# Kernel tuning notes

Hardware: AMD Instinct MI355X
Metric: run time of the kernel (lower is better)

## Reference

```python
import jax, jax.numpy as jnp
import numpy as np

N_NODES = 200_000
BRANCH = 8      # n: one-hot width / max children encoded
K_DEPTH = 16    # k: number of stacked levels, h_emb = n*k


def setup_inputs() -> dict:
    b, N = BRANCH, N_NODES
    idx = np.arange(N, dtype=np.int64)
    # complete b-ary forest (single tree): parent of node i is (i-1)//b
    parent = np.maximum((idx - 1) // b, 0)
    child_idx = np.where(idx > 0, (idx - 1) % b, 0)
    # depth via level start offsets of a complete b-ary tree
    starts = np.array([(b ** d - 1) // (b - 1) for d in range(K_DEPTH + 1)], dtype=np.int64)
    depth = (np.searchsorted(starts, idx, side='right') - 1).astype(np.int32)
    # p_emb buffer: p**i with p = 1.0 (unused by the original forward)
    p_emb = jnp.ones((BRANCH * K_DEPTH,), dtype=jnp.float32)
    return {
        'parent': jnp.asarray(parent, jnp.int32),
        'child_idx': jnp.asarray(child_idx, jnp.int32),
        'depth': jnp.asarray(depth, jnp.int32),
        'p_emb': p_emb,
        'n': BRANCH,
        'k': K_DEPTH,
    }


def reference(parent, child_idx, depth, p_emb, n, k):
    """Level-parallel tree positional embedding.

    Original per-node loop: child.pos[n:] = parent.pos[:-n]; child.pos[:n] = eye_row.
    Equivalent top-down level sweep: at level d, every node takes its parent's
    embedding shifted right by n slots and prepends the one-hot of its sibling
    index (one_hot yields zeros for child_idx >= n, matching torch.eye rows).
    """
    N = parent.shape[0]
    h = n * k
    onehot = jax.nn.one_hot(child_idx, n, dtype=jnp.float32)  # [N, n]

    def body(d, emb):
        par = emb[parent]                                      # [N, h] gather
        shifted = jnp.concatenate([onehot, par[:, : h - n]], axis=1)
        return jnp.where((depth == d)[:, None], shifted, emb)

    emb0 = jnp.zeros((N, h), dtype=jnp.float32)                # roots stay zero
    pos_embeds = jax.lax.fori_loop(1, k + 1, body, emb0)
    return pos_embeds
```

## Files before the change

kernel.cpp:

```cpp
#include <hip/hip_runtime.h>


#define PE_K 16
#define ROWS_PER_BLOCK 128

__global__ __launch_bounds__(256) void PositionalEmbedding_kernel(
    const int* __restrict__ parent,
    const int* __restrict__ child_idx,
    const int* __restrict__ depth,
    float* __restrict__ out,
    int N) {
  __shared__ unsigned long long codes[ROWS_PER_BLOCK];

  const int tid  = threadIdx.x;
  const int row0 = blockIdx.x * ROWS_PER_BLOCK;

  if (tid < ROWS_PER_BLOCK) {
    int row = row0 + tid;
    unsigned long long code = 0;
    if (row < N) {
      int d  = depth[row];
      int dd = d < PE_K ? d : PE_K;
      int cur = row;
      for (int j = 0; j < dd; ++j) {
        int ci = child_idx[cur] & 7;
        code |= (unsigned long long)ci << (3 * j);
        cur = parent[cur];
      }
      code |= (unsigned long long)dd << 48;
    }
    codes[tid] = code;
  }
  __syncthreads();

  const int c  = tid & 31;
  const int g  = tid >> 5;
  const int j  = c >> 1;
  const int sh = 3 * j;
  const int r0 = 4 * c - 8 * j;

  float4* p = reinterpret_cast<float4*>(out) + ((long long)(row0 + g) * 32 + c);
  const int last_full_rl = N - row0;

  #pragma unroll
  for (int it = 0; it < ROWS_PER_BLOCK / 8; ++it) {
    int rl = it * 8 + g;
    unsigned long long code = codes[rl];
    int dd = (int)(code >> 48);
    int ci = (int)((code >> sh) & 7);
    ci = (j < dd) ? ci : 8;

    float4 v;
    v.x = (ci == r0 + 0) ? 1.f : 0.f;
    v.y = (ci == r0 + 1) ? 1.f : 0.f;
    v.z = (ci == r0 + 2) ? 1.f : 0.f;
    v.w = (ci == r0 + 3) ? 1.f : 0.f;

    if (rl < last_full_rl) *p = v;
    p += 8 * 32;
  }
}

extern "C" void kernel_launch(void* const* d_in, const int* in_sizes, int n_in,
                              void* d_out, int out_size, void* d_ws, size_t ws_size,
                              hipStream_t stream) {
  const int* parent    = (const int*)d_in[0];
  const int* child_idx = (const int*)d_in[1];
  const int* depth     = (const int*)d_in[2];
  float* out = (float*)d_out;
  int N = in_sizes[0];

  int grid = (N + ROWS_PER_BLOCK - 1) / ROWS_PER_BLOCK;
  PositionalEmbedding_kernel<<<grid, 256, 0, stream>>>(parent, child_idx, depth, out, N);
}
```

Measured before the change: 21.62 us.

## Compute codes per wave and broadcast via shuffles, use nontemporal stores

Each wave now builds path codes for its 64 rows and distributes them with wave shuffles, replacing the shared-memory buffer and block barrier. All threads now take part in the ancestor walk instead of half, and codes use 4-bit fields with a sentinel of 8, so the depth field is no longer needed. Output writes become nontemporal vector stores, which avoids polluting the cache with the write-only embedding. The cost is two shuffles per output row instead of one LDS read.

```diff
diff --git a/kernel.cpp b/kernel.cpp
--- a/kernel.cpp
+++ b/kernel.cpp
@@ -2,7 +2,8 @@
 
 
 #define PE_K 16
-#define ROWS_PER_BLOCK 128
+
+typedef float vf4 __attribute__((ext_vector_type(4)));
 
 __global__ __launch_bounds__(256) void PositionalEmbedding_kernel(
     const int* __restrict__ parent,
@@ -10,54 +11,52 @@
     const int* __restrict__ depth,
     float* __restrict__ out,
     int N) {
-  __shared__ unsigned long long codes[ROWS_PER_BLOCK];
+  const int lane = threadIdx.x & 63;
+  const int wave = threadIdx.x >> 6;
+  const long long base = (long long)blockIdx.x * 256 + (long long)wave * 64;
 
-  const int tid  = threadIdx.x;
-  const int row0 = blockIdx.x * ROWS_PER_BLOCK;
-
-  if (tid < ROWS_PER_BLOCK) {
-    int row = row0 + tid;
-    unsigned long long code = 0;
-    if (row < N) {
+  unsigned long long code = 0x8888888888888888ULL;
+  {
+    int row = (int)base + lane;
+    if (base < N && row < N) {
       int d  = depth[row];
       int dd = d < PE_K ? d : PE_K;
       int cur = row;
       for (int j = 0; j < dd; ++j) {
-        int ci = child_idx[cur] & 7;
-        code |= (unsigned long long)ci << (3 * j);
+        unsigned long long ci = (unsigned long long)(child_idx[cur] & 7);
+        code = (code & ~(0xFULL << (4 * j))) | (ci << (4 * j));
         cur = parent[cur];
       }
-      code |= (unsigned long long)dd << 48;
     }
-    codes[tid] = code;
   }
-  __syncthreads();
+  unsigned int clo = (unsigned int)code;
+  unsigned int chi = (unsigned int)(code >> 32);
 
-  const int c  = tid & 31;
-  const int g  = tid >> 5;
+  const int c  = lane & 31;
+  const int g  = lane >> 5;
   const int j  = c >> 1;
-  const int sh = 3 * j;
+  const int sh = 4 * j;
   const int r0 = 4 * c - 8 * j;
 
-  float4* p = reinterpret_cast<float4*>(out) + ((long long)(row0 + g) * 32 + c);
-  const int last_full_rl = N - row0;
+  vf4* p = reinterpret_cast<vf4*>(out) + (base + g) * 32 + c;
+  const long long limit = (long long)N - base;
 
   #pragma unroll
-  for (int it = 0; it < ROWS_PER_BLOCK / 8; ++it) {
-    int rl = it * 8 + g;
-    unsigned long long code = codes[rl];
-    int dd = (int)(code >> 48);
-    int ci = (int)((code >> sh) & 7);
-    ci = (j < dd) ? ci : 8;
+  for (int it = 0; it < 32; ++it) {
+    int rl = it * 2 + g;
+    unsigned int lo = __shfl(clo, rl);
+    unsigned int hi = __shfl(chi, rl);
+    unsigned long long cc = ((unsigned long long)hi << 32) | lo;
+    int ci = (int)((cc >> sh) & 15);
 
-    float4 v;
+    vf4 v;
     v.x = (ci == r0 + 0) ? 1.f : 0.f;
     v.y = (ci == r0 + 1) ? 1.f : 0.f;
     v.z = (ci == r0 + 2) ? 1.f : 0.f;
     v.w = (ci == r0 + 3) ? 1.f : 0.f;
 
-    if (rl < last_full_rl) *p = v;
-    p += 8 * 32;
+    if (rl < limit) __builtin_nontemporal_store(v, p);
+    p += 2 * 32;
   }
 }
 
@@ -70,6 +69,6 @@
   float* out = (float*)d_out;
   int N = in_sizes[0];
 
-  int grid = (N + ROWS_PER_BLOCK - 1) / ROWS_PER_BLOCK;
+  int grid = (N + 255) / 256;
   PositionalEmbedding_kernel<<<grid, 256, 0, stream>>>(parent, child_idx, depth, out, N);
 }
```

Result: slower. 24.07 us (+11.3%).
